# Optimization experiments

Measured on AMD Instinct MI355X. Metric: run time of the kernel, lower is better.

The kernel has to match this reference:

```python
import jax, jax.numpy as jnp
import numpy as np

B, N, D = 4, 4096, 512
H = 8
HD = D // H  # 64


def setup_inputs() -> dict:
    key = jax.random.key(0)
    ks = jax.random.split(key, 9)
    s = 1.0 / np.sqrt(D)
    return {
        "x": jax.random.normal(ks[0], (B, N, D), dtype=jnp.float32),
        "Wq": jax.random.normal(ks[1], (D, D), dtype=jnp.float32) * s,
        "bq": jax.random.normal(ks[2], (D,), dtype=jnp.float32) * 0.01,
        "Wk": jax.random.normal(ks[3], (D, D), dtype=jnp.float32) * s,
        "bk": jax.random.normal(ks[4], (D,), dtype=jnp.float32) * 0.01,
        "Wv": jax.random.normal(ks[5], (D, D), dtype=jnp.float32) * s,
        "bv": jax.random.normal(ks[6], (D,), dtype=jnp.float32) * 0.01,
        "Wo": jax.random.normal(ks[7], (D, D), dtype=jnp.float32) * s,
        "bo": jax.random.normal(ks[8], (D,), dtype=jnp.float32) * 0.01,
    }


def reference(x, Wq, bq, Wk, bk, Wv, bv, Wo, bo):
    # projections -> [B, H, N, HD]
    def split_heads(t):
        return t.reshape(B, N, H, HD).transpose(0, 2, 1, 3)

    q = split_heads(x @ Wq.T + bq)
    k = split_heads(x @ Wk.T + bk)
    v = split_heads(x @ Wv.T + bv)

    scale = 1.0 / np.sqrt(HD).astype(np.float32)
    scores = jnp.einsum("bhqd,bhkd->bhqk", q, k) * scale  # [B,H,N,N]
    attn = jax.nn.softmax(scores, axis=-1)
    out = jnp.einsum("bhqk,bhkd->bhqd", attn, v)  # [B,H,N,HD]
    out = out.transpose(0, 2, 1, 3).reshape(B, N, D)
    return out @ Wo.T + bo
```

## Files before the change

kernel.cpp:

```cpp
#include <hip/hip_runtime.h>
#include <hip/hip_bf16.h>

#define BB 4
#define NN 4096
#define DD 512
#define HH 8
#define HD 64

typedef __attribute__((ext_vector_type(4))) float f32x4;
typedef __attribute__((ext_vector_type(16))) float f32x16;
typedef __attribute__((ext_vector_type(8))) short short8;
typedef __attribute__((ext_vector_type(4))) unsigned int uint4v;

static __device__ __forceinline__ unsigned short f2bf(float f) {
    unsigned int u = __float_as_uint(f);
    u += 0x7fff + ((u >> 16) & 1);
    return (unsigned short)(u >> 16);
}

__global__ void convert_bf16(const float* __restrict__ in,
                             unsigned short* __restrict__ out, int n) {
    int i = (blockIdx.x * blockDim.x + threadIdx.x) * 8;
    int stride = gridDim.x * blockDim.x * 8;
    for (; i + 7 < n; i += stride) {
        f32x4 a = *reinterpret_cast<const f32x4*>(in + i);
        f32x4 b = *reinterpret_cast<const f32x4*>(in + i + 4);
        short8 o;
        o[0] = (short)f2bf(a[0]); o[1] = (short)f2bf(a[1]);
        o[2] = (short)f2bf(a[2]); o[3] = (short)f2bf(a[3]);
        o[4] = (short)f2bf(b[0]); o[5] = (short)f2bf(b[1]);
        o[6] = (short)f2bf(b[2]); o[7] = (short)f2bf(b[3]);
        *reinterpret_cast<short8*>(out + i) = o;
    }
}

__global__ void convert_weights(const float* __restrict__ W0, const float* __restrict__ W1,
                                const float* __restrict__ W2, const float* __restrict__ W3,
                                unsigned short* __restrict__ out) {
    int which = blockIdx.x >> 7;
    const float* src = which == 0 ? W0 : which == 1 ? W1 : which == 2 ? W2 : W3;
    unsigned short* dst = out + (size_t)which * DD * DD;
    int i = ((blockIdx.x & 127) * blockDim.x + threadIdx.x) * 8;
    f32x4 a = *reinterpret_cast<const f32x4*>(src + i);
    f32x4 b = *reinterpret_cast<const f32x4*>(src + i + 4);
    short8 o;
    o[0] = (short)f2bf(a[0]); o[1] = (short)f2bf(a[1]);
    o[2] = (short)f2bf(a[2]); o[3] = (short)f2bf(a[3]);
    o[4] = (short)f2bf(b[0]); o[5] = (short)f2bf(b[1]);
    o[6] = (short)f2bf(b[2]); o[7] = (short)f2bf(b[3]);
    *reinterpret_cast<short8*>(dst + i) = o;
}

template <int OUT_MODE>
__device__ __forceinline__
void gemm_tile(const unsigned short* __restrict__ A,
               const unsigned short* __restrict__ W,
               const float* __restrict__ bias,
               void* __restrict__ Cout, float scale,
               int brow, int bcol, uint4* ldsA, uint4* ldsB) {
    const int t = threadIdx.x;
    const int lane = t & 63;
    const int w = t >> 6;
    const int wr = w >> 1, wc = w & 1;
    const int l16 = lane & 15;
    const int lq = lane >> 4;

    f32x4 acc[4][4] = {};

    const int sr = t >> 1;
    const int c16 = (t & 1) * 2;

    for (int k0 = 0; k0 < 512; k0 += 32) {
        const uint4* gA = reinterpret_cast<const uint4*>(A + (size_t)(brow + sr) * 512 + k0 + c16 * 8);
        const uint4* gB = reinterpret_cast<const uint4*>(W + (size_t)(bcol + sr) * 512 + k0 + c16 * 8);
        uint4 a0 = gA[0], a1 = gA[1];
        uint4 b0 = gB[0], b1 = gB[1];
        __syncthreads();
        ldsA[(sr * 4 + c16) ^ (sr & 7)]     = a0;
        ldsA[(sr * 4 + c16 + 1) ^ (sr & 7)] = a1;
        ldsB[(sr * 4 + c16) ^ (sr & 7)]     = b0;
        ldsB[(sr * 4 + c16 + 1) ^ (sr & 7)] = b1;
        __syncthreads();
        short8 af[4], bfr[4];
#pragma unroll
        for (int m = 0; m < 4; ++m) {
            int ra = wr * 64 + m * 16 + l16;
            af[m] = *reinterpret_cast<short8*>(&ldsA[(ra * 4 + lq) ^ (ra & 7)]);
            int rb = wc * 64 + m * 16 + l16;
            bfr[m] = *reinterpret_cast<short8*>(&ldsB[(rb * 4 + lq) ^ (rb & 7)]);
        }
#pragma unroll
        for (int m = 0; m < 4; ++m)
#pragma unroll
            for (int n = 0; n < 4; ++n)
                acc[m][n] = __builtin_amdgcn_mfma_f32_16x16x32_bf16(af[m], bfr[n], acc[m][n], 0, 0, 0);
    }

#pragma unroll
    for (int m = 0; m < 4; ++m) {
        int row = brow + wr * 64 + m * 16 + lq * 4;
#pragma unroll
        for (int n = 0; n < 4; ++n) {
            int col = bcol + wc * 64 + n * 16 + l16;
            float bv = bias[col];
            if (OUT_MODE == 2) {
                int bh = ((row >> 12) << 3) + (col >> 6);
                int d = col & 63;
                int ntok = row & 4095;
                ushort4 o;
                o.x = f2bf(acc[m][n][0] + bv);
                o.y = f2bf(acc[m][n][1] + bv);
                o.z = f2bf(acc[m][n][2] + bv);
                o.w = f2bf(acc[m][n][3] + bv);
                *reinterpret_cast<ushort4*>(
                    (unsigned short*)Cout + ((size_t)bh * 64 + d) * 4096 + ntok) = o;
            } else {
#pragma unroll
                for (int r = 0; r < 4; ++r) {
                    float v = (acc[m][n][r] + bv) * scale;
                    if (OUT_MODE == 1) {
                        ((unsigned short*)Cout)[(size_t)(row + r) * 512 + col] = f2bf(v);
                    } else {
                        ((float*)Cout)[(size_t)(row + r) * 512 + col] = v;
                    }
                }
            }
        }
    }
}

__global__ __launch_bounds__(256)
void gemm_qkv(const unsigned short* __restrict__ xb,
              const unsigned short* __restrict__ Wall,
              const float* __restrict__ bq, const float* __restrict__ bk,
              const float* __restrict__ bv,
              unsigned short* __restrict__ Qb, unsigned short* __restrict__ Kb,
              unsigned short* __restrict__ Vt, float cl) {
    __shared__ uint4 ldsA[128 * 4];
    __shared__ uint4 ldsB[128 * 4];
    int z = blockIdx.z;
    const unsigned short* W = Wall + (size_t)z * DD * DD;
    int brow = (int)blockIdx.y * 128, bcol = (int)blockIdx.x * 128;
    if (z == 0) {
        gemm_tile<1>(xb, W, bq, Qb, cl, brow, bcol, ldsA, ldsB);
    } else if (z == 1) {
        gemm_tile<1>(xb, W, bk, Kb, 1.0f, brow, bcol, ldsA, ldsB);
    } else {
        gemm_tile<2>(xb, W, bv, Vt, 1.0f, brow, bcol, ldsA, ldsB);
    }
}

__global__ __launch_bounds__(256)
void gemm_bias_f32(const unsigned short* __restrict__ A,
                   const unsigned short* __restrict__ W,
                   const float* __restrict__ bias,
                   float* __restrict__ Cout) {
    __shared__ uint4 ldsA[128 * 4];
    __shared__ uint4 ldsB[128 * 4];
    gemm_tile<0>(A, W, bias, Cout, 1.0f,
                 (int)blockIdx.y * 128, (int)blockIdx.x * 128, ldsA, ldsB);
}

__global__ __launch_bounds__(128)
void flash_attn(const unsigned short* __restrict__ Qb,
                const unsigned short* __restrict__ Kb,
                const unsigned short* __restrict__ Vt,
                unsigned short* __restrict__ Ob) {
    __shared__ __align__(16) char lds[32768];
    const int t = threadIdx.x;
    const int lane = t & 63;
    const int w = t >> 6;
    const int nid = (blockIdx.x & 7) * 256 + (blockIdx.x >> 3);
    const int bh = nid >> 6;
    const int qb = nid & 63;
    const int b = bh >> 3, h = bh & 7;
    const int q0 = qb * 64 + w * 32;
    const int l32 = lane & 31;
    const int hi = lane >> 5;

    const int i8 = lane >> 3, g8 = lane & 7;

    const unsigned short* qptr = Qb + (size_t)(b * NN + q0 + l32) * DD + h * HD + hi * 8;
    short8 qf[4];
#pragma unroll
    for (int c = 0; c < 4; ++c)
        qf[c] = *reinterpret_cast<const short8*>(qptr + c * 16);

    const f32x16 Z = {};
    f32x16 OT0 = {}, OT1 = {};
    float lsum = 0.f;

    int koff[8], voff[8];
#pragma unroll
    for (int sub = 0; sub < 2; ++sub) {
#pragma unroll
        for (int c = 0; c < 4; ++c) {
            int row = sub * 32 + l32;
            int g = (hi + 2 * c) ^ (row & 7) ^ ((row >> 3) & 7);
            koff[sub * 4 + c] = row * 128 + g * 16;
        }
#pragma unroll
        for (int dblk = 0; dblk < 2; ++dblk)
#pragma unroll
            for (int c2 = 0; c2 < 2; ++c2) {
                int row = dblk * 32 + l32;
                int g = ((sub << 2) + (c2 << 1) + hi) ^ (row & 7) ^ ((row >> 3) & 7);
                voff[sub * 4 + dblk * 2 + c2] = 8192 + row * 128 + g * 16;
            }
    }

    const unsigned short* kp[4];
    const unsigned short* vp[4];
#pragma unroll
    for (int jj = 0; jj < 4; ++jj) {
        int rl = w * 32 + jj * 8 + i8;
        int gk = (g8 ^ i8 ^ ((w * 4 + jj) & 7)) * 8;
        kp[jj] = Kb + (size_t)(b * NN + rl) * DD + h * HD + gk;
        vp[jj] = Vt + ((size_t)bh * HD + rl) * NN + gk;
    }

    auto STAGE = [&](int bb) {
#pragma unroll
        for (int jj = 0; jj < 4; ++jj) {
            __builtin_amdgcn_global_load_lds(
                (const __attribute__((address_space(1))) void*)kp[jj],
                (__attribute__((address_space(3))) void*)(lds + bb + (w * 32 + jj * 8) * 128), 16, 0, 0);
            kp[jj] += 64 * DD;
        }
#pragma unroll
        for (int jj = 0; jj < 4; ++jj) {
            __builtin_amdgcn_global_load_lds(
                (const __attribute__((address_space(1))) void*)vp[jj],
                (__attribute__((address_space(3))) void*)(lds + bb + 8192 + (w * 32 + jj * 8) * 128), 16, 0, 0);
            vp[jj] += 64;
        }
    };

    auto softpack = [&](const f32x16& S, short8& pa, short8& pb) {
        unsigned int wq[8];
#pragma unroll
        for (int j = 0; j < 8; ++j) {
            float p0 = __builtin_exp2f(S[2 * j]);
            float p1 = __builtin_exp2f(S[2 * j + 1]);
            lsum += p0 + p1;
            asm("v_cvt_pk_bf16_f32 %0, %1, %2" : "=v"(wq[j]) : "v"(p0), "v"(p1));
        }
        asm("v_permlane32_swap_b32 %0, %1" : "+v"(wq[0]), "+v"(wq[2]));
        asm("v_permlane32_swap_b32 %0, %1" : "+v"(wq[1]), "+v"(wq[3]));
        asm("v_permlane32_swap_b32 %0, %1" : "+v"(wq[4]), "+v"(wq[6]));
        asm("v_permlane32_swap_b32 %0, %1" : "+v"(wq[5]), "+v"(wq[7]));
        uint4v pu0 = {wq[0], wq[1], wq[2], wq[3]};
        uint4v pu1 = {wq[4], wq[5], wq[6], wq[7]};
        pa = __builtin_bit_cast(short8, pu0);
        pb = __builtin_bit_cast(short8, pu1);
    };

    auto COMPUTE = [&](int BO) {
#pragma unroll
        for (int sub = 0; sub < 2; ++sub) {
            short8 kf0 = *reinterpret_cast<const short8*>(lds + BO + koff[sub * 4 + 0]);
            short8 kf1 = *reinterpret_cast<const short8*>(lds + BO + koff[sub * 4 + 1]);
            short8 kf2 = *reinterpret_cast<const short8*>(lds + BO + koff[sub * 4 + 2]);
            short8 kf3 = *reinterpret_cast<const short8*>(lds + BO + koff[sub * 4 + 3]);
            f32x16 S;
            S = __builtin_amdgcn_mfma_f32_32x32x16_bf16(kf0, qf[0], Z, 0, 0, 0);
            S = __builtin_amdgcn_mfma_f32_32x32x16_bf16(kf1, qf[1], S, 0, 0, 0);
            S = __builtin_amdgcn_mfma_f32_32x32x16_bf16(kf2, qf[2], S, 0, 0, 0);
            S = __builtin_amdgcn_mfma_f32_32x32x16_bf16(kf3, qf[3], S, 0, 0, 0);
            short8 vf0 = *reinterpret_cast<const short8*>(lds + BO + voff[sub * 4 + 0]);
            short8 vf1 = *reinterpret_cast<const short8*>(lds + BO + voff[sub * 4 + 1]);
            short8 vf2 = *reinterpret_cast<const short8*>(lds + BO + voff[sub * 4 + 2]);
            short8 vf3 = *reinterpret_cast<const short8*>(lds + BO + voff[sub * 4 + 3]);
            short8 pa, pb;
            softpack(S, pa, pb);
            OT0 = __builtin_amdgcn_mfma_f32_32x32x16_bf16(vf0, pa, OT0, 0, 0, 0);
            OT0 = __builtin_amdgcn_mfma_f32_32x32x16_bf16(vf1, pb, OT0, 0, 0, 0);
            OT1 = __builtin_amdgcn_mfma_f32_32x32x16_bf16(vf2, pa, OT1, 0, 0, 0);
            OT1 = __builtin_amdgcn_mfma_f32_32x32x16_bf16(vf3, pb, OT1, 0, 0, 0);
        }
    };

    STAGE(0);
    asm volatile("s_waitcnt vmcnt(0)" ::: "memory");
    __builtin_amdgcn_s_barrier();
    asm volatile("" ::: "memory");

    for (int it = 0; it < 32; ++it) {
        STAGE(16384);
        asm volatile("s_waitcnt vmcnt(8)" ::: "memory");
        __builtin_amdgcn_s_barrier();
        asm volatile("" ::: "memory");
        COMPUTE(0);
        asm volatile("" ::: "memory");
        __builtin_amdgcn_s_barrier();
        asm volatile("" ::: "memory");
        if (it != 31) {
            STAGE(0);
            asm volatile("s_waitcnt vmcnt(8)" ::: "memory");
        } else {
            asm volatile("s_waitcnt vmcnt(0)" ::: "memory");
        }
        __builtin_amdgcn_s_barrier();
        asm volatile("" ::: "memory");
        COMPUTE(16384);
        if (it != 31) {
            asm volatile("" ::: "memory");
            __builtin_amdgcn_s_barrier();
            asm volatile("" ::: "memory");
        }
    }

    lsum += __shfl_xor(lsum, 32);
    float inv = 1.0f / lsum;
    char* lw = lds + w * 4096;
#pragma unroll
    for (int dblk = 0; dblk < 2; ++dblk) {
#pragma unroll
        for (int g = 0; g < 4; ++g) {
#pragma unroll
            for (int j = 0; j < 2; ++j) {
                int r = 4 * g + 2 * j;
                int d = dblk * 32 + 8 * g + 2 * j + 4 * hi;
                float a = (dblk ? OT1[r] : OT0[r]) * inv;
                float bqv = (dblk ? OT1[r + 1] : OT0[r + 1]) * inv;
                unsigned int wv;
                asm("v_cvt_pk_bf16_f32 %0, %1, %2" : "=v"(wv) : "v"(a), "v"(bqv));
                int addr = (l32 * 128 + d * 2) ^ ((l32 & 7) << 4);
                *reinterpret_cast<unsigned int*>(lw + addr) = wv;
            }
        }
    }
#pragma unroll
    for (int it = 0; it < 4; ++it) {
        int q = lane >> 1;
        int seg = (lane & 1) + it * 2;
        uint4 val = *reinterpret_cast<uint4*>(lw + ((q * 128 + seg * 16) ^ ((q & 7) << 4)));
        *reinterpret_cast<uint4*>(Ob + (size_t)(b * NN + q0 + q) * DD + h * HD + seg * 8) = val;
    }
}

extern "C" void kernel_launch(void* const* d_in, const int* in_sizes, int n_in,
                              void* d_out, int out_size, void* d_ws, size_t ws_size,
                              hipStream_t stream) {
    (void)in_sizes; (void)n_in; (void)out_size; (void)ws_size;
    const float* x  = (const float*)d_in[0];
    const float* Wq = (const float*)d_in[1];
    const float* bq = (const float*)d_in[2];
    const float* Wk = (const float*)d_in[3];
    const float* bk = (const float*)d_in[4];
    const float* Wv = (const float*)d_in[5];
    const float* bv = (const float*)d_in[6];
    const float* Wo = (const float*)d_in[7];
    const float* bo = (const float*)d_in[8];
    float* out = (float*)d_out;

    char* ws = (char*)d_ws;
    const size_t BUF = 16777216;
    unsigned short* xb  = (unsigned short*)(ws);
    unsigned short* Qb  = (unsigned short*)(ws + BUF);
    unsigned short* Kb  = (unsigned short*)(ws + 2 * BUF);
    unsigned short* Vt  = (unsigned short*)(ws + 3 * BUF);
    unsigned short* Wqb = (unsigned short*)(ws + 4 * BUF);
    unsigned short* Wob = Wqb + 3 * 262144;
    unsigned short* Ob  = xb;

    const int NTOK = BB * NN;
    const float cl = 0.125f * 1.4426950408889634f;

    convert_bf16<<<2048, 256, 0, stream>>>(x, xb, NTOK * DD);
    convert_weights<<<512, 256, 0, stream>>>(Wq, Wk, Wv, Wo, Wqb);

    dim3 ggrid(4, NTOK / 128, 3);
    gemm_qkv<<<ggrid, 256, 0, stream>>>(xb, Wqb, bq, bk, bv, Qb, Kb, Vt, cl);

    flash_attn<<<2048, 128, 0, stream>>>(Qb, Kb, Vt, Ob);

    gemm_bias_f32<<<dim3(4, NTOK / 128), 256, 0, stream>>>(Ob, Wob, bo, out);
}
```

Baseline: 322.0 us.

## Enlarge flash-attention block to four waves sharing each staged K/V tile

The attention kernel now launches 256-thread blocks covering 128 queries instead of 128-thread blocks covering 64. All four waves share the same double-buffered K/V tile in LDS, so each wave issues half as many global-to-LDS loads, and the wait counts are adjusted to match. The goal is to halve K/V staging traffic per query. In exchange there are half as many blocks, each holding more waves at its barriers, and the launch bounds now ask for three blocks per CU, which can change register allocation.

```diff
diff --git a/kernel.cpp b/kernel.cpp
--- a/kernel.cpp
+++ b/kernel.cpp
@@ -161,7 +161,7 @@
                  (int)blockIdx.y * 128, (int)blockIdx.x * 128, ldsA, ldsB);
 }
 
-__global__ __launch_bounds__(128)
+__global__ __launch_bounds__(256, 3)
 void flash_attn(const unsigned short* __restrict__ Qb,
                 const unsigned short* __restrict__ Kb,
                 const unsigned short* __restrict__ Vt,
@@ -170,11 +170,11 @@
     const int t = threadIdx.x;
     const int lane = t & 63;
     const int w = t >> 6;
-    const int nid = (blockIdx.x & 7) * 256 + (blockIdx.x >> 3);
-    const int bh = nid >> 6;
-    const int qb = nid & 63;
+    const int nid = (blockIdx.x & 7) * 128 + (blockIdx.x >> 3);
+    const int bh = nid >> 5;
+    const int qb = nid & 31;
     const int b = bh >> 3, h = bh & 7;
-    const int q0 = qb * 64 + w * 32;
+    const int q0 = qb * 128 + w * 32;
     const int l32 = lane & 31;
     const int hi = lane >> 5;
 
@@ -209,31 +209,29 @@
             }
     }
 
-    const unsigned short* kp[4];
-    const unsigned short* vp[4];
-#pragma unroll
-    for (int jj = 0; jj < 4; ++jj) {
-        int rl = w * 32 + jj * 8 + i8;
-        int gk = (g8 ^ i8 ^ ((w * 4 + jj) & 7)) * 8;
-        kp[jj] = Kb + (size_t)(b * NN + rl) * DD + h * HD + gk;
-        vp[jj] = Vt + ((size_t)bh * HD + rl) * NN + gk;
-    }
+    const int rowl0 = w * 16 + i8;
+    const int rowl1 = w * 16 + 8 + i8;
+    const int gs0 = (g8 ^ i8 ^ ((2 * w) & 7)) * 8;
+    const int gs1 = (g8 ^ i8 ^ ((2 * w + 1) & 7)) * 8;
+    const unsigned short* kp0 = Kb + (size_t)(b * NN + rowl0) * DD + h * HD + gs0;
+    const unsigned short* kp1 = Kb + (size_t)(b * NN + rowl1) * DD + h * HD + gs1;
+    const unsigned short* vp0 = Vt + ((size_t)bh * HD + rowl0) * NN + gs0;
+    const unsigned short* vp1 = Vt + ((size_t)bh * HD + rowl1) * NN + gs1;
 
     auto STAGE = [&](int bb) {
-#pragma unroll
-        for (int jj = 0; jj < 4; ++jj) {
-            __builtin_amdgcn_global_load_lds(
-                (const __attribute__((address_space(1))) void*)kp[jj],
-                (__attribute__((address_space(3))) void*)(lds + bb + (w * 32 + jj * 8) * 128), 16, 0, 0);
-            kp[jj] += 64 * DD;
-        }
-#pragma unroll
-        for (int jj = 0; jj < 4; ++jj) {
-            __builtin_amdgcn_global_load_lds(
-                (const __attribute__((address_space(1))) void*)vp[jj],
-                (__attribute__((address_space(3))) void*)(lds + bb + 8192 + (w * 32 + jj * 8) * 128), 16, 0, 0);
-            vp[jj] += 64;
-        }
+        __builtin_amdgcn_global_load_lds(
+            (const __attribute__((address_space(1))) void*)kp0,
+            (__attribute__((address_space(3))) void*)(lds + bb + (w * 16) * 128), 16, 0, 0);
+        __builtin_amdgcn_global_load_lds(
+            (const __attribute__((address_space(1))) void*)kp1,
+            (__attribute__((address_space(3))) void*)(lds + bb + (w * 16 + 8) * 128), 16, 0, 0);
+        __builtin_amdgcn_global_load_lds(
+            (const __attribute__((address_space(1))) void*)vp0,
+            (__attribute__((address_space(3))) void*)(lds + bb + 8192 + (w * 16) * 128), 16, 0, 0);
+        __builtin_amdgcn_global_load_lds(
+            (const __attribute__((address_space(1))) void*)vp1,
+            (__attribute__((address_space(3))) void*)(lds + bb + 8192 + (w * 16 + 8) * 128), 16, 0, 0);
+        kp0 += 64 * DD; kp1 += 64 * DD; vp0 += 64; vp1 += 64;
     };
 
     auto softpack = [&](const f32x16& S, short8& pa, short8& pb) {
@@ -287,7 +285,7 @@
 
     for (int it = 0; it < 32; ++it) {
         STAGE(16384);
-        asm volatile("s_waitcnt vmcnt(8)" ::: "memory");
+        asm volatile("s_waitcnt vmcnt(4)" ::: "memory");
         __builtin_amdgcn_s_barrier();
         asm volatile("" ::: "memory");
         COMPUTE(0);
@@ -296,7 +294,7 @@
         asm volatile("" ::: "memory");
         if (it != 31) {
             STAGE(0);
-            asm volatile("s_waitcnt vmcnt(8)" ::: "memory");
+            asm volatile("s_waitcnt vmcnt(4)" ::: "memory");
         } else {
             asm volatile("s_waitcnt vmcnt(0)" ::: "memory");
         }
@@ -373,7 +371,7 @@
     dim3 ggrid(4, NTOK / 128, 3);
     gemm_qkv<<<ggrid, 256, 0, stream>>>(xb, Wqb, bq, bk, bv, Qb, Kb, Vt, cl);
 
-    flash_attn<<<2048, 128, 0, stream>>>(Qb, Kb, Vt, Ob);
+    flash_attn<<<1024, 256, 0, stream>>>(Qb, Kb, Vt, Ob);
 
     gemm_bias_f32<<<dim3(4, NTOK / 128), 256, 0, stream>>>(Ob, Wob, bo, out);
 }
```

Measured after the change: 269.9 us (median of 2 runs). 16.2% less time.
